# Kernel tuning notes

Hardware: AMD Instinct MI355X
Metric: run time of the kernel (lower is better)

## Reference

```python
import jax, jax.numpy as jnp
import numpy as np

G = 16          # groups
K = 5           # kernel_size
IPG = 1024 // G # in_channels_per_group
OPG = 1024 // G # out_channels_per_group


def setup_inputs() -> dict:
    key = jax.random.key(0)
    k1, k2, k3 = jax.random.split(key, 3)
    inputs = jax.random.normal(k1, (4, 4096, 1024), dtype=jnp.float32)
    positions = jnp.sort(
        jax.random.randint(k2, (4, 4096), 0, 8192, dtype=jnp.int32), axis=-1)
    # kaiming-uniform-like init for kernel [G, OPG, IPG, K]
    fan_in = IPG * K
    bound = float(np.sqrt(6.0 / fan_in))
    kernel = jax.random.uniform(k3, (G, OPG, IPG, K), dtype=jnp.float32,
                                minval=-bound, maxval=bound)
    return {"inputs": inputs, "positions": positions, "kernel": kernel}


def reference(inputs, positions, kernel):
    B, L, C = inputs.shape
    c = K // 2
    # pad sequence dim; pad positions with -1 sentinel (never matches expected)
    pi = jnp.pad(inputs, ((0, 0), (c, c), (0, 0)))            # [B, L+2c, C]
    pp = jnp.pad(positions, ((0, 0), (c, c)), constant_values=-1)  # [B, L+2c]
    # sliding-window gather indices (equivalent to unfold with stride 1)
    idx = jnp.arange(L)[:, None] + jnp.arange(K)[None, :]      # [L, K]
    ip = pi[:, idx, :]        # [B, L, K, C] input patches
    ppatch = pp[:, idx]       # [B, L, K]  position patches
    # center of each patch is the original position at that output index
    offsets = jnp.arange(-c, c + 1, dtype=positions.dtype)    # [K]
    expected = positions[:, :, None] + offsets                # [B, L, K]
    mask = (ppatch == expected).astype(inputs.dtype)          # [B, L, K]
    masked = ip * mask[..., None]                             # [B, L, K, C]
    # split channels into groups: [B, L, K, G, IPG]
    gp = masked.reshape(B, L, K, G, IPG)
    # grouped conv reduce over in_channels_per_group and kernel taps
    out = jnp.einsum('blkgi,goik->blgo', gp, kernel)           # [B, L, G, OPG]
    return out
```

## Files before the change

kernel.cpp:

```cpp
#include <hip/hip_runtime.h>

typedef __attribute__((ext_vector_type(8))) short short8;
typedef __attribute__((ext_vector_type(4))) float float4v;
typedef __attribute__((ext_vector_type(4))) unsigned short us4;

namespace {
constexpr int NG   = 16;
constexpr int LSEQ = 4096;
constexpr int CIN  = 1024;
constexpr int IPG  = 64;
constexpr int OPG  = 64;
constexpr int KT   = 5;
constexpr int ROWS_PER_CHUNK = 128;
constexpr int CHUNKS = 4;
constexpr int ROWS_PER_BLOCK = ROWS_PER_CHUNK * CHUNKS;
constexpr int SW_STRIDE  = 328;
constexpr int SIN_STRIDE = 72;
constexpr int SIN_ROWS   = ROWS_PER_CHUNK + KT - 1;
}

__device__ __forceinline__ unsigned short f2bf(float f) {
  unsigned int u = __builtin_bit_cast(unsigned int, f);
  u += 0x7fffu + ((u >> 16) & 1u);
  return (unsigned short)(u >> 16);
}

__global__ __launch_bounds__(256, 2) void mconv_f32_mfma(
    const float* __restrict__ gin,
    const int* __restrict__ gpos,
    const float* __restrict__ gwt,
    float* __restrict__ gout) {
  __shared__ __align__(16) unsigned short sW[OPG * SW_STRIDE];
  __shared__ __align__(16) unsigned short sIn[SIN_ROWS * SIN_STRIDE];
  __shared__ unsigned char sMask[ROWS_PER_CHUNK * KT];

  const int tid  = threadIdx.x;
  const int wave = tid >> 6;
  const int lane = tid & 63;
  const int quad = lane >> 4;
  const int l16  = lane & 15;

  const int g  = blockIdx.y;
  const int b  = blockIdx.z;
  const int tile0 = blockIdx.x * ROWS_PER_BLOCK;
  const int bL = b * LSEQ;

  {
    const float* wg = gwt + (size_t)g * (OPG * IPG * KT);
    for (int u = tid; u < (OPG * IPG * KT) / 4; u += 256) {
      const int base = u * 4;
      float4v v = *(const float4v*)(wg + base);
      int o = base / (IPG * KT);
      int r = base - o * (IPG * KT);
      int i = r / KT;
      int k = r - i * KT;
      int addr = o * SW_STRIDE + k * IPG + i;
      #pragma unroll
      for (int t = 0; t < 4; ++t) {
        sW[addr] = f2bf(v[t]);
        ++k; addr += IPG;
        if (k == KT) { k = 0; ++i; addr -= KT * IPG - 1; }
      }
    }
  }

  const short8 zero8 = {0, 0, 0, 0, 0, 0, 0, 0};
  const float4v zf = {0.f, 0.f, 0.f, 0.f};

  for (int ch = 0; ch < CHUNKS; ++ch) {
    const int l0 = tile0 + ch * ROWS_PER_CHUNK;
    __syncthreads();

    for (int t = tid; t < ROWS_PER_CHUNK * KT; t += 256) {
      const int lr  = t / KT;
      const int tap = t - lr * KT;
      const int l   = l0 + lr;
      const int lsrc = l + tap - 2;
      int ok = 0;
      if (lsrc >= 0 && lsrc < LSEQ)
        ok = (gpos[bL + lsrc] == gpos[bL + l] + (tap - 2));
      sMask[t] = (unsigned char)ok;
    }

    for (int u = tid; u < SIN_ROWS * 16; u += 256) {
      const int r  = u >> 4;
      const int c4 = u & 15;
      const int l  = l0 - 2 + r;
      us4 w = {0, 0, 0, 0};
      if (l >= 0 && l < LSEQ) {
        float4v v = *(const float4v*)(gin + (size_t)(bL + l) * CIN + g * IPG + c4 * 4);
        w[0] = f2bf(v[0]); w[1] = f2bf(v[1]); w[2] = f2bf(v[2]); w[3] = f2bf(v[3]);
      }
      *(us4*)(&sIn[r * SIN_STRIDE + c4 * 4]) = w;
    }
    __syncthreads();

    float4v acc[2][4];
    #pragma unroll
    for (int mm = 0; mm < 2; ++mm)
      #pragma unroll
      for (int nt = 0; nt < 4; ++nt)
        acc[mm][nt] = zf;

    const int m0 = wave * 32 + l16;
    const int m1 = m0 + 16;

    #pragma unroll
    for (int tap = 0; tap < KT; ++tap) {
      const bool msk0 = sMask[m0 * KT + tap] != 0;
      const bool msk1 = sMask[m1 * KT + tap] != 0;
      #pragma unroll
      for (int h = 0; h < 2; ++h) {
        const int kk = tap * IPG + h * 32 + quad * 8;
        const short8 b0 = *(const short8*)(&sW[(0 * 16 + l16) * SW_STRIDE + kk]);
        const short8 b1 = *(const short8*)(&sW[(1 * 16 + l16) * SW_STRIDE + kk]);
        const short8 b2 = *(const short8*)(&sW[(2 * 16 + l16) * SW_STRIDE + kk]);
        const short8 b3 = *(const short8*)(&sW[(3 * 16 + l16) * SW_STRIDE + kk]);
        const int ci = h * 32 + quad * 8;
        short8 a0 = *(const short8*)(&sIn[(m0 + tap) * SIN_STRIDE + ci]);
        short8 a1 = *(const short8*)(&sIn[(m1 + tap) * SIN_STRIDE + ci]);
        if (!msk0) a0 = zero8;
        if (!msk1) a1 = zero8;
        acc[0][0] = __builtin_amdgcn_mfma_f32_16x16x32_bf16(a0, b0, acc[0][0], 0, 0, 0);
        acc[0][1] = __builtin_amdgcn_mfma_f32_16x16x32_bf16(a0, b1, acc[0][1], 0, 0, 0);
        acc[0][2] = __builtin_amdgcn_mfma_f32_16x16x32_bf16(a0, b2, acc[0][2], 0, 0, 0);
        acc[0][3] = __builtin_amdgcn_mfma_f32_16x16x32_bf16(a0, b3, acc[0][3], 0, 0, 0);
        acc[1][0] = __builtin_amdgcn_mfma_f32_16x16x32_bf16(a1, b0, acc[1][0], 0, 0, 0);
        acc[1][1] = __builtin_amdgcn_mfma_f32_16x16x32_bf16(a1, b1, acc[1][1], 0, 0, 0);
        acc[1][2] = __builtin_amdgcn_mfma_f32_16x16x32_bf16(a1, b2, acc[1][2], 0, 0, 0);
        acc[1][3] = __builtin_amdgcn_mfma_f32_16x16x32_bf16(a1, b3, acc[1][3], 0, 0, 0);
      }
    }

    #pragma unroll
    for (int mm = 0; mm < 2; ++mm) {
      const int lrow = l0 + wave * 32 + mm * 16 + quad * 4;
      #pragma unroll
      for (int reg = 0; reg < 4; ++reg) {
        float* orow = gout + ((size_t)(bL + lrow + reg) * NG + g) * OPG;
        #pragma unroll
        for (int nt = 0; nt < 4; ++nt)
          orow[nt * 16 + l16] = acc[mm][nt][reg];
      }
    }
  }
}

extern "C" void kernel_launch(void* const* d_in, const int* in_sizes, int n_in,
                              void* d_out, int out_size, void* d_ws, size_t ws_size,
                              hipStream_t stream) {
  (void)in_sizes; (void)n_in; (void)out_size; (void)d_ws; (void)ws_size;
  const float* gin  = (const float*)d_in[0];
  const int*   gpos = (const int*)d_in[1];
  const float* gwt  = (const float*)d_in[2];
  float*       gout = (float*)d_out;
  dim3 grid(LSEQ / ROWS_PER_BLOCK, NG, 4);
  dim3 block(256);
  hipLaunchKernelGGL(mconv_f32_mfma, grid, block, 0, stream,
                     gin, gpos, gwt, gout);
}
```

Baseline: 149.9 us.

## Pre-swizzle weights into MFMA fragments in workspace; drop per-block weight staging

Adds a small prep kernel that converts the weights to bf16 once and stores them in MFMA B-fragment order in the workspace. The main kernel then streams weight fragments straight from global/L2 with a one-step prefetch instead of rebuilding a transposed copy in shared memory in every block. The main kernel also moves to 128-row blocks with a 2x2 wave tiling, packs the mask into bits, swizzles the sIn layout to avoid bank conflicts, and raises occupancy. The old kernel stays as a fallback when the workspace is too small. In exchange it adds a second launch and a weight-prep pass on every call.

```diff
diff --git a/kernel.cpp b/kernel.cpp
--- a/kernel.cpp
+++ b/kernel.cpp
@@ -11,12 +11,12 @@
 constexpr int IPG  = 64;
 constexpr int OPG  = 64;
 constexpr int KT   = 5;
-constexpr int ROWS_PER_CHUNK = 128;
-constexpr int CHUNKS = 4;
-constexpr int ROWS_PER_BLOCK = ROWS_PER_CHUNK * CHUNKS;
-constexpr int SW_STRIDE  = 328;
+constexpr int ROWS = 128;
 constexpr int SIN_STRIDE = 72;
-constexpr int SIN_ROWS   = ROWS_PER_CHUNK + KT - 1;
+constexpr int SIN_ROWS   = ROWS + KT - 1;
+constexpr int KSTEPS = 10;
+constexpr size_t WFRAG_SHORTS = (size_t)NG * 4 * KSTEPS * 512;
+constexpr size_t WFRAG_BYTES  = WFRAG_SHORTS * 2;
 }
 
 __device__ __forceinline__ unsigned short f2bf(float f) {
@@ -25,13 +25,144 @@
   return (unsigned short)(u >> 16);
 }
 
-__global__ __launch_bounds__(256, 2) void mconv_f32_mfma(
+__global__ __launch_bounds__(256) void wprep(const float* __restrict__ gwt,
+                                             unsigned short* __restrict__ wfrag) {
+  const int u = blockIdx.x * 256 + threadIdx.x;
+  const int E    = u * 8;
+  const int tile = E >> 9;
+  const int w9   = E & 511;
+  const int n    = w9 >> 5;
+  const int quad = (w9 & 31) >> 3;
+  const int ks   = tile % KSTEPS;
+  const int tt   = tile / KSTEPS;
+  const int t    = tt & 3;
+  const int g    = tt >> 2;
+  const int tap  = ks >> 1;
+  const int h    = ks & 1;
+  const int o    = t * 16 + n;
+  const float* src = gwt + (((size_t)(g * 64 + o) * 64) + h * 32 + quad * 8) * KT + tap;
+  short8 v;
+  #pragma unroll
+  for (int j = 0; j < 8; ++j)
+    v[j] = (short)f2bf(src[j * KT]);
+  *(short8*)(wfrag + E) = v;
+}
+
+__global__ __launch_bounds__(256, 4) void mconv_main(
     const float* __restrict__ gin,
     const int* __restrict__ gpos,
-    const float* __restrict__ gwt,
+    const unsigned short* __restrict__ wfrag,
     float* __restrict__ gout) {
+  __shared__ __align__(16) unsigned short sIn[SIN_ROWS * SIN_STRIDE];
+  __shared__ unsigned char sMaskB[ROWS];
+
+  const int tid  = threadIdx.x;
+  const int wv   = tid >> 6;
+  const int lane = tid & 63;
+  const int quad = lane >> 4;
+  const int l16  = lane & 15;
+  const int wm   = wv & 1;
+  const int wn   = wv >> 1;
+
+  const int g  = blockIdx.y;
+  const int b  = blockIdx.z;
+  const int l0 = blockIdx.x * ROWS;
+  const int bL = b * LSEQ;
+
+  for (int u = tid; u < SIN_ROWS * 16; u += 256) {
+    const int r  = u >> 4;
+    const int c4 = u & 15;
+    const int l  = l0 - 2 + r;
+    us4 w = {0, 0, 0, 0};
+    if (l >= 0 && l < LSEQ) {
+      float4v v = *(const float4v*)(gin + (size_t)(bL + l) * CIN + g * IPG + c4 * 4);
+      w[0] = f2bf(v[0]); w[1] = f2bf(v[1]); w[2] = f2bf(v[2]); w[3] = f2bf(v[3]);
+    }
+    const int p = (c4 * 4 + ((r & 3) << 4)) & 63;
+    *(us4*)(&sIn[r * SIN_STRIDE + p]) = w;
+  }
+
+  if (tid < ROWS) {
+    const int l = l0 + tid;
+    const int pc = gpos[bL + l];
+    unsigned int mbits = 0;
+    #pragma unroll
+    for (int tap = 0; tap < KT; ++tap) {
+      const int lsrc = l + tap - 2;
+      int ok = 0;
+      if (lsrc >= 0 && lsrc < LSEQ)
+        ok = (gpos[bL + lsrc] == pc + (tap - 2));
+      mbits |= (unsigned int)ok << tap;
+    }
+    sMaskB[tid] = (unsigned char)mbits;
+  }
+  __syncthreads();
+
+  int mb[4];
+  #pragma unroll
+  for (int mt = 0; mt < 4; ++mt)
+    mb[mt] = sMaskB[wm * 64 + mt * 16 + l16];
+
+  const int laneoff = l16 * 32 + quad * 8;
+  const unsigned short* wb0 = wfrag + (size_t)((g * 4 + wn * 2) * KSTEPS) * 512 + laneoff;
+  const unsigned short* wb1 = wb0 + (size_t)KSTEPS * 512;
+
+  const short8 zero8 = {0, 0, 0, 0, 0, 0, 0, 0};
+  const float4v zf = {0.f, 0.f, 0.f, 0.f};
+  float4v acc[4][2];
+  #pragma unroll
+  for (int mt = 0; mt < 4; ++mt) { acc[mt][0] = zf; acc[mt][1] = zf; }
+
+  short8 bc0 = *(const short8*)(wb0);
+  short8 bc1 = *(const short8*)(wb1);
+
+  #pragma unroll 2
+  for (int ks = 0; ks < KSTEPS; ++ks) {
+    const int ksn = (ks + 1 < KSTEPS) ? ks + 1 : KSTEPS - 1;
+    short8 bn0 = *(const short8*)(wb0 + ksn * 512);
+    short8 bn1 = *(const short8*)(wb1 + ksn * 512);
+    const int tap = ks >> 1;
+    const int h   = ks & 1;
+    const int s   = h * 32 + quad * 8;
+    #pragma unroll
+    for (int mt = 0; mt < 4; ++mt) {
+      const int r  = wm * 64 + mt * 16 + l16 + tap;
+      const int sp = (s + ((r & 3) << 4)) & 63;
+      short8 a = *(const short8*)(&sIn[r * SIN_STRIDE + sp]);
+      if (!((mb[mt] >> tap) & 1)) a = zero8;
+      acc[mt][0] = __builtin_amdgcn_mfma_f32_16x16x32_bf16(a, bc0, acc[mt][0], 0, 0, 0);
+      acc[mt][1] = __builtin_amdgcn_mfma_f32_16x16x32_bf16(a, bc1, acc[mt][1], 0, 0, 0);
+    }
+    bc0 = bn0; bc1 = bn1;
+  }
+
+  #pragma unroll
+  for (int mt = 0; mt < 4; ++mt) {
+    const int lrow = l0 + wm * 64 + mt * 16 + quad * 4;
+    #pragma unroll
+    for (int reg = 0; reg < 4; ++reg) {
+      float* orow = gout + (size_t)(bL + lrow + reg) * CIN + g * OPG + wn * 32;
+      orow[l16]      = acc[mt][0][reg];
+      orow[16 + l16] = acc[mt][1][reg];
+    }
+  }
+}
+
+namespace fb {
+constexpr int ROWS_PER_CHUNK = 128;
+constexpr int CHUNKS = 4;
+constexpr int ROWS_PER_BLOCK = 512;
+constexpr int SW_STRIDE  = 328;
+constexpr int FSIN_STRIDE = 72;
+constexpr int FSIN_ROWS   = 132;
+}
+
+__global__ __launch_bounds__(256, 2) void mconv_f32_mfma(
+    const float* __restrict__ gin, const int* __restrict__ gpos,
+    const float* __restrict__ gwt, float* __restrict__ gout) {
+  using namespace fb;
   __shared__ __align__(16) unsigned short sW[OPG * SW_STRIDE];
-  __shared__ __align__(16) unsigned short sIn[SIN_ROWS * SIN_STRIDE];
+  __shared__ __align__(16) unsigned short sIn[FSIN_ROWS * FSIN_STRIDE];
   __shared__ unsigned char sMask[ROWS_PER_CHUNK * KT];
 
   const int tid  = threadIdx.x;
@@ -39,7 +170,6 @@
   const int lane = tid & 63;
   const int quad = lane >> 4;
   const int l16  = lane & 15;
-
   const int g  = blockIdx.y;
   const int b  = blockIdx.z;
   const int tile0 = blockIdx.x * ROWS_PER_BLOCK;
@@ -63,48 +193,33 @@
       }
     }
   }
-
-  const short8 zero8 = {0, 0, 0, 0, 0, 0, 0, 0};
-  const float4v zf = {0.f, 0.f, 0.f, 0.f};
-
+  const short8 zero8 = {0,0,0,0,0,0,0,0};
+  const float4v zf = {0.f,0.f,0.f,0.f};
   for (int ch = 0; ch < CHUNKS; ++ch) {
     const int l0 = tile0 + ch * ROWS_PER_CHUNK;
     __syncthreads();
-
     for (int t = tid; t < ROWS_PER_CHUNK * KT; t += 256) {
-      const int lr  = t / KT;
-      const int tap = t - lr * KT;
-      const int l   = l0 + lr;
-      const int lsrc = l + tap - 2;
+      const int lr = t / KT, tap = t - lr * KT, l = l0 + lr, lsrc = l + tap - 2;
       int ok = 0;
-      if (lsrc >= 0 && lsrc < LSEQ)
-        ok = (gpos[bL + lsrc] == gpos[bL + l] + (tap - 2));
+      if (lsrc >= 0 && lsrc < LSEQ) ok = (gpos[bL + lsrc] == gpos[bL + l] + (tap - 2));
       sMask[t] = (unsigned char)ok;
     }
-
-    for (int u = tid; u < SIN_ROWS * 16; u += 256) {
-      const int r  = u >> 4;
-      const int c4 = u & 15;
-      const int l  = l0 - 2 + r;
-      us4 w = {0, 0, 0, 0};
+    for (int u = tid; u < FSIN_ROWS * 16; u += 256) {
+      const int r = u >> 4, c4 = u & 15, l = l0 - 2 + r;
+      us4 w = {0,0,0,0};
       if (l >= 0 && l < LSEQ) {
         float4v v = *(const float4v*)(gin + (size_t)(bL + l) * CIN + g * IPG + c4 * 4);
-        w[0] = f2bf(v[0]); w[1] = f2bf(v[1]); w[2] = f2bf(v[2]); w[3] = f2bf(v[3]);
-      }
-      *(us4*)(&sIn[r * SIN_STRIDE + c4 * 4]) = w;
+        w[0]=f2bf(v[0]); w[1]=f2bf(v[1]); w[2]=f2bf(v[2]); w[3]=f2bf(v[3]);
+      }
+      *(us4*)(&sIn[r * FSIN_STRIDE + c4 * 4]) = w;
     }
     __syncthreads();
-
     float4v acc[2][4];
     #pragma unroll
     for (int mm = 0; mm < 2; ++mm)
       #pragma unroll
-      for (int nt = 0; nt < 4; ++nt)
-        acc[mm][nt] = zf;
-
-    const int m0 = wave * 32 + l16;
-    const int m1 = m0 + 16;
-
+      for (int nt = 0; nt < 4; ++nt) acc[mm][nt] = zf;
+    const int m0 = wave * 32 + l16, m1 = m0 + 16;
     #pragma unroll
     for (int tap = 0; tap < KT; ++tap) {
       const bool msk0 = sMask[m0 * KT + tap] != 0;
@@ -112,26 +227,25 @@
       #pragma unroll
       for (int h = 0; h < 2; ++h) {
         const int kk = tap * IPG + h * 32 + quad * 8;
-        const short8 b0 = *(const short8*)(&sW[(0 * 16 + l16) * SW_STRIDE + kk]);
-        const short8 b1 = *(const short8*)(&sW[(1 * 16 + l16) * SW_STRIDE + kk]);
-        const short8 b2 = *(const short8*)(&sW[(2 * 16 + l16) * SW_STRIDE + kk]);
-        const short8 b3 = *(const short8*)(&sW[(3 * 16 + l16) * SW_STRIDE + kk]);
+        const short8 b0 = *(const short8*)(&sW[(0*16 + l16) * SW_STRIDE + kk]);
+        const short8 b1 = *(const short8*)(&sW[(1*16 + l16) * SW_STRIDE + kk]);
+        const short8 b2 = *(const short8*)(&sW[(2*16 + l16) * SW_STRIDE + kk]);
+        const short8 b3 = *(const short8*)(&sW[(3*16 + l16) * SW_STRIDE + kk]);
         const int ci = h * 32 + quad * 8;
-        short8 a0 = *(const short8*)(&sIn[(m0 + tap) * SIN_STRIDE + ci]);
-        short8 a1 = *(const short8*)(&sIn[(m1 + tap) * SIN_STRIDE + ci]);
+        short8 a0 = *(const short8*)(&sIn[(m0 + tap) * FSIN_STRIDE + ci]);
+        short8 a1 = *(const short8*)(&sIn[(m1 + tap) * FSIN_STRIDE + ci]);
         if (!msk0) a0 = zero8;
         if (!msk1) a1 = zero8;
-        acc[0][0] = __builtin_amdgcn_mfma_f32_16x16x32_bf16(a0, b0, acc[0][0], 0, 0, 0);
-        acc[0][1] = __builtin_amdgcn_mfma_f32_16x16x32_bf16(a0, b1, acc[0][1], 0, 0, 0);
-        acc[0][2] = __builtin_amdgcn_mfma_f32_16x16x32_bf16(a0, b2, acc[0][2], 0, 0, 0);
-        acc[0][3] = __builtin_amdgcn_mfma_f32_16x16x32_bf16(a0, b3, acc[0][3], 0, 0, 0);
-        acc[1][0] = __builtin_amdgcn_mfma_f32_16x16x32_bf16(a1, b0, acc[1][0], 0, 0, 0);
-        acc[1][1] = __builtin_amdgcn_mfma_f32_16x16x32_bf16(a1, b1, acc[1][1], 0, 0, 0);
-        acc[1][2] = __builtin_amdgcn_mfma_f32_16x16x32_bf16(a1, b2, acc[1][2], 0, 0, 0);
-        acc[1][3] = __builtin_amdgcn_mfma_f32_16x16x32_bf16(a1, b3, acc[1][3], 0, 0, 0);
-      }
-    }
-
+        acc[0][0] = __builtin_amdgcn_mfma_f32_16x16x32_bf16(a0,b0,acc[0][0],0,0,0);
+        acc[0][1] = __builtin_amdgcn_mfma_f32_16x16x32_bf16(a0,b1,acc[0][1],0,0,0);
+        acc[0][2] = __builtin_amdgcn_mfma_f32_16x16x32_bf16(a0,b2,acc[0][2],0,0,0);
+        acc[0][3] = __builtin_amdgcn_mfma_f32_16x16x32_bf16(a0,b3,acc[0][3],0,0,0);
+        acc[1][0] = __builtin_amdgcn_mfma_f32_16x16x32_bf16(a1,b0,acc[1][0],0,0,0);
+        acc[1][1] = __builtin_amdgcn_mfma_f32_16x16x32_bf16(a1,b1,acc[1][1],0,0,0);
+        acc[1][2] = __builtin_amdgcn_mfma_f32_16x16x32_bf16(a1,b2,acc[1][2],0,0,0);
+        acc[1][3] = __builtin_amdgcn_mfma_f32_16x16x32_bf16(a1,b3,acc[1][3],0,0,0);
+      }
+    }
     #pragma unroll
     for (int mm = 0; mm < 2; ++mm) {
       const int lrow = l0 + wave * 32 + mm * 16 + quad * 4;
@@ -149,13 +263,21 @@
 extern "C" void kernel_launch(void* const* d_in, const int* in_sizes, int n_in,
                               void* d_out, int out_size, void* d_ws, size_t ws_size,
                               hipStream_t stream) {
-  (void)in_sizes; (void)n_in; (void)out_size; (void)d_ws; (void)ws_size;
+  (void)in_sizes; (void)n_in; (void)out_size;
   const float* gin  = (const float*)d_in[0];
   const int*   gpos = (const int*)d_in[1];
   const float* gwt  = (const float*)d_in[2];
   float*       gout = (float*)d_out;
-  dim3 grid(LSEQ / ROWS_PER_BLOCK, NG, 4);
-  dim3 block(256);
-  hipLaunchKernelGGL(mconv_f32_mfma, grid, block, 0, stream,
-                     gin, gpos, gwt, gout);
-}
+
+  if (ws_size >= WFRAG_BYTES) {
+    unsigned short* wfrag = (unsigned short*)d_ws;
+    hipLaunchKernelGGL(wprep, dim3(160), dim3(256), 0, stream, gwt, wfrag);
+    dim3 grid(LSEQ / ROWS, NG, 4);
+    hipLaunchKernelGGL(mconv_main, grid, dim3(256), 0, stream,
+                       gin, gpos, wfrag, gout);
+  } else {
+    dim3 grid(LSEQ / fb::ROWS_PER_BLOCK, NG, 4);
+    hipLaunchKernelGGL(mconv_f32_mfma, grid, dim3(256), 0, stream,
+                       gin, gpos, gwt, gout);
+  }
+}
```

Measured after the change: 132.4 us. 11.7% less time.
